# Kernel tuning notes

Hardware: AMD Instinct MI355X
Metric: run time of the kernel (lower is better)

## Reference

```python
import jax, jax.numpy as jnp
import numpy as np


def setup_inputs() -> dict:
    key = jax.random.key(0)
    k1, k2, k3, k4 = jax.random.split(key, 4)
    B, N, F, T, K, O = 16, 1024, 16, 12, 3, 16
    x = jax.random.normal(k1, (B, N, F, T), dtype=jnp.float32)
    spatial_attention = jax.random.uniform(k2, (B, N, N), dtype=jnp.float32)
    adj = jax.random.uniform(k3, (N, N), dtype=jnp.float32)
    # xavier_uniform_ on [K, F, O]: bound = sqrt(6/(F+O)) over last two dims
    bound = float(np.sqrt(6.0 / (F + O)))
    Theta = jax.random.uniform(k4, (K, F, O), dtype=jnp.float32, minval=-bound, maxval=bound)
    return {"x": x, "spatial_attention": spatial_attention, "adj": adj, "Theta": Theta}


def reference(x, spatial_attention, adj, Theta):
    # x: [B, N, F, T], spatial_attention: [B, N, N], adj: [N, N], Theta: [K, F, O]
    B, N, F, T = x.shape
    K = Theta.shape[0]
    a = adj[None, :, :] * spatial_attention                      # [B, N, N]
    eye = jnp.broadcast_to(jnp.eye(N, dtype=x.dtype), (B, N, N))
    supports = [eye, a]
    for _ in range(2, K):                                        # power series of adjacency
        supports.append(jnp.matmul(supports[-1], a))
    S = jnp.stack(supports, axis=0)                              # [K, B, N, N]
    # rhs[k,b,n,f,t] = sum_m S[k,b,m,n] * x[b,m,f,t]  (supports[k]^T @ x), fused over T and K
    rhs = jnp.einsum('kbmn,bmft->kbnft', S, x)                   # [K, B, N, F, T]
    out = jnp.einsum('kbnft,kfo->bnot', rhs, Theta)              # [B, N, O, T]
    return jax.nn.relu(out)
```

## Files before the change

### kernel.cpp

```cpp
#include <hip/hip_runtime.h>
#include <hip/hip_bf16.h>


typedef __attribute__((ext_vector_type(8))) __bf16 bf16x8;
typedef __attribute__((ext_vector_type(4))) float  f32x4;
typedef __attribute__((ext_vector_type(8))) short  short8;

__device__ inline unsigned short f32_to_bf16(float f) {
    unsigned int u = __builtin_bit_cast(unsigned int, f);
    unsigned int r = u + 0x7FFFu + ((u >> 16) & 1u);
    return (unsigned short)(r >> 16);
}
__device__ inline float bf16_to_f32(unsigned short u) {
    unsigned int x = ((unsigned int)u) << 16;
    return __builtin_bit_cast(float, x);
}

__global__ void prep_a(const float* __restrict__ sa, const float* __restrict__ adj,
                       unsigned short* __restrict__ aT)
{
    __shared__ float tile[32][33];
    const int b  = blockIdx.z;
    const int m0 = blockIdx.y * 32;
    const int n0 = blockIdx.x * 32;
    const int tid = threadIdx.x;
    const int c  = tid & 31;
    const int r4 = tid >> 5;
    const float* sab = sa + (size_t)b * 1024 * 1024;
#pragma unroll
    for (int i = 0; i < 4; i++) {
        int rr = r4 + i * 8;
        size_t idx = (size_t)(m0 + rr) * 1024 + (n0 + c);
        tile[rr][c] = adj[idx] * sab[idx];
    }
    __syncthreads();
    unsigned short* aTb = aT + (size_t)b * 1024 * 1024;
#pragma unroll
    for (int i = 0; i < 4; i++) {
        int rr = r4 + i * 8;
        aTb[(size_t)(n0 + rr) * 1024 + (m0 + c)] = f32_to_bf16(tile[c][rr]);
    }
}

__global__ void prep_x(const float* __restrict__ x, unsigned short* __restrict__ xT)
{
    __shared__ float tile[32][33];
    const int b  = blockIdx.z;
    const int j0 = blockIdx.y * 32;
    const int m0 = blockIdx.x * 32;
    const int tid = threadIdx.x;
    const int c  = tid & 31;
    const int r4 = tid >> 5;
    const float* xb = x + (size_t)b * 1024 * 192;
#pragma unroll
    for (int i = 0; i < 4; i++) {
        int rr = r4 + i * 8;
        tile[rr][c] = xb[(size_t)(m0 + rr) * 192 + (j0 + c)];
    }
    __syncthreads();
    unsigned short* xTb = xT + (size_t)b * 192 * 1024;
#pragma unroll
    for (int i = 0; i < 4; i++) {
        int rr = r4 + i * 8;
        xTb[(size_t)(j0 + rr) * 1024 + (m0 + c)] = f32_to_bf16(tile[c][rr]);
    }
}

#define GEMM_BJ 96
#define GEMM_BN 128
#define GEMM_BK 64
#define LDS_STRIDE 72

__global__ __launch_bounds__(256, 2)
void gemm_tn(const unsigned short* __restrict__ Aop,
             const unsigned short* __restrict__ Bop,
             unsigned short* __restrict__ Cout)
{
    const int b  = blockIdx.z;
    const int j0 = blockIdx.y * GEMM_BJ;
    const int n0 = blockIdx.x * GEMM_BN;
    const unsigned short* Ab = Aop + (size_t)b * 192 * 1024;
    const unsigned short* Bb = Bop + (size_t)b * 1024 * 1024;

    __shared__ unsigned short Alds[GEMM_BJ][LDS_STRIDE];
    __shared__ unsigned short Blds[GEMM_BN][LDS_STRIDE];

    const int tid  = threadIdx.x;
    const int lane = tid & 63;
    const int wave = tid >> 6;
    const int wj   = wave >> 1;
    const int wn   = wave & 1;
    const int lr   = lane & 15;
    const int lk   = (lane >> 4) * 8;

    f32x4 acc[3][4];
#pragma unroll
    for (int i = 0; i < 3; i++)
#pragma unroll
        for (int j = 0; j < 4; j++) acc[i][j] = f32x4{0.f, 0.f, 0.f, 0.f};

    for (int m0 = 0; m0 < 1024; m0 += GEMM_BK) {
        short8 aval[3], bval[4];
#pragma unroll
        for (int i = 0; i < 3; i++) {
            int id = tid + i * 256, r = id >> 3, c = id & 7;
            aval[i] = *reinterpret_cast<const short8*>(Ab + (size_t)(j0 + r) * 1024 + m0 + c * 8);
        }
#pragma unroll
        for (int i = 0; i < 4; i++) {
            int id = tid + i * 256, r = id >> 3, c = id & 7;
            bval[i] = *reinterpret_cast<const short8*>(Bb + (size_t)(n0 + r) * 1024 + m0 + c * 8);
        }
        __syncthreads();
#pragma unroll
        for (int i = 0; i < 3; i++) {
            int id = tid + i * 256, r = id >> 3, c = id & 7;
            *reinterpret_cast<short8*>(&Alds[r][c * 8]) = aval[i];
        }
#pragma unroll
        for (int i = 0; i < 4; i++) {
            int id = tid + i * 256, r = id >> 3, c = id & 7;
            *reinterpret_cast<short8*>(&Blds[r][c * 8]) = bval[i];
        }
        __syncthreads();
#pragma unroll
        for (int kk = 0; kk < GEMM_BK; kk += 32) {
            bf16x8 af[3], bfr[4];
#pragma unroll
            for (int ri = 0; ri < 3; ri++)
                af[ri] = __builtin_bit_cast(bf16x8,
                    *reinterpret_cast<const short8*>(&Alds[wj * 48 + ri * 16 + lr][kk + lk]));
#pragma unroll
            for (int ci = 0; ci < 4; ci++)
                bfr[ci] = __builtin_bit_cast(bf16x8,
                    *reinterpret_cast<const short8*>(&Blds[wn * 64 + ci * 16 + lr][kk + lk]));
#pragma unroll
            for (int ri = 0; ri < 3; ri++)
#pragma unroll
                for (int ci = 0; ci < 4; ci++)
                    acc[ri][ci] = __builtin_amdgcn_mfma_f32_16x16x32_bf16(
                        af[ri], bfr[ci], acc[ri][ci], 0, 0, 0);
        }
    }
    unsigned short* Cb = Cout + (size_t)b * 192 * 1024;
    const int jw = j0 + wj * 48;
    const int nw = n0 + wn * 64;
#pragma unroll
    for (int ri = 0; ri < 3; ri++)
#pragma unroll
        for (int ci = 0; ci < 4; ci++) {
            int col = nw + ci * 16 + lr;
#pragma unroll
            for (int r = 0; r < 4; r++) {
                int row = jw + ri * 16 + (lane >> 4) * 4 + r;
                Cb[(size_t)row * 1024 + col] = f32_to_bf16(acc[ri][ci][r]);
            }
        }
}

__global__ __launch_bounds__(256)
void final_contract(const unsigned short* __restrict__ xT,
                    const unsigned short* __restrict__ r1,
                    const unsigned short* __restrict__ r2,
                    const float* __restrict__ Theta,
                    float* __restrict__ out)
{
    __shared__ float th[3][16][16];
    const int tid = threadIdx.x;
    for (int i = tid; i < 768; i += 256) ((float*)th)[i] = Theta[i];
    __syncthreads();

    const int gid = blockIdx.x * 256 + tid;
    const int n   = gid & 1023;
    const int btq = gid >> 10;
    const int tq  = btq % 3;
    const int b   = btq / 3;
    const size_t base = (size_t)b * 192 * 1024 + n;

    float acc[4][16];
#pragma unroll
    for (int tt = 0; tt < 4; tt++)
#pragma unroll
        for (int o = 0; o < 16; o++) acc[tt][o] = 0.f;

#pragma unroll
    for (int f = 0; f < 16; f++) {
        size_t off = base + (size_t)(f * 12 + tq * 4) * 1024;
        float v0[4], v1[4], v2[4];
#pragma unroll
        for (int tt = 0; tt < 4; tt++) {
            v0[tt] = bf16_to_f32(xT[off + (size_t)tt * 1024]);
            v1[tt] = bf16_to_f32(r1[off + (size_t)tt * 1024]);
            v2[tt] = bf16_to_f32(r2[off + (size_t)tt * 1024]);
        }
        const f32x4* t0 = reinterpret_cast<const f32x4*>(&th[0][f][0]);
        const f32x4* t1 = reinterpret_cast<const f32x4*>(&th[1][f][0]);
        const f32x4* t2 = reinterpret_cast<const f32x4*>(&th[2][f][0]);
#pragma unroll
        for (int q = 0; q < 4; q++) {
            f32x4 w0 = t0[q], w1 = t1[q], w2 = t2[q];
#pragma unroll
            for (int tt = 0; tt < 4; tt++)
#pragma unroll
                for (int e = 0; e < 4; e++)
                    acc[tt][q * 4 + e] += v0[tt] * w0[e] + v1[tt] * w1[e] + v2[tt] * w2[e];
        }
    }
    float* outp = out + ((size_t)(b * 1024 + n) * 16) * 12 + tq * 4;
#pragma unroll
    for (int o = 0; o < 16; o++) {
        f32x4 v;
#pragma unroll
        for (int tt = 0; tt < 4; tt++) v[tt] = fmaxf(acc[tt][o], 0.f);
        *reinterpret_cast<f32x4*>(&outp[o * 12]) = v;
    }
}

extern "C" void kernel_launch(void* const* d_in, const int* in_sizes, int n_in,
                              void* d_out, int out_size, void* d_ws, size_t ws_size,
                              hipStream_t stream)
{
    const float* x     = (const float*)d_in[0];
    const float* sa    = (const float*)d_in[1];
    const float* adj   = (const float*)d_in[2];
    const float* Theta = (const float*)d_in[3];
    float* out = (float*)d_out;

    char* ws = (char*)d_ws;
    const size_t SZ_AT = (size_t)16 * 1024 * 1024 * 2;
    const size_t SZ_XT = (size_t)16 * 192  * 1024 * 2;
    unsigned short* aT = (unsigned short*)ws;
    unsigned short* xT = (unsigned short*)(ws + SZ_AT);
    unsigned short* r1 = (unsigned short*)(ws + SZ_AT + SZ_XT);
    unsigned short* r2 = (unsigned short*)(ws + SZ_AT + 2 * SZ_XT);

    prep_a<<<dim3(32, 32, 16), 256, 0, stream>>>(sa, adj, aT);
    prep_x<<<dim3(32, 6, 16), 256, 0, stream>>>(x, xT);
    gemm_tn<<<dim3(8, 2, 16), 256, 0, stream>>>(xT, aT, r1);
    gemm_tn<<<dim3(8, 2, 16), 256, 0, stream>>>(r1, aT, r2);
    final_contract<<<dim3(192), 256, 0, stream>>>(xT, r1, r2, Theta, out);
}
```

Measured before the change: 85.18 us.

## Double-buffer GEMM with direct global-to-LDS loads and stage output via LDS

The batched GEMM now streams the adjacency operand into double-buffered, XOR-swizzled LDS using global_load_lds, and keeps the A operand in registers loaded straight from global memory with prefetch of the next K-step. This removes the register round trip and one barrier per iteration. The N tile drops from 128 to 64, doubling the grid. The final contraction is regrouped per 64 nodes and stages its ReLU output in LDS so it can write fully coalesced f32x4 stores. The cost is 48KB of LDS in final_contract, one idle wave out of four there, and more redundant A-operand loads per GEMM block.

```diff
diff --git a/kernel.cpp b/kernel.cpp
--- a/kernel.cpp
+++ b/kernel.cpp
@@ -14,6 +14,13 @@
 __device__ inline float bf16_to_f32(unsigned short u) {
     unsigned int x = ((unsigned int)u) << 16;
     return __builtin_bit_cast(float, x);
+}
+
+__device__ inline void gload_lds16(const void* gsrc, void* ldst) {
+    __builtin_amdgcn_global_load_lds(
+        (const __attribute__((address_space(1))) unsigned int*)gsrc,
+        (__attribute__((address_space(3))) unsigned int*)ldst,
+        16, 0, 0);
 }
 
 __global__ void prep_a(const float* __restrict__ sa, const float* __restrict__ adj,
@@ -66,24 +73,18 @@
     }
 }
 
-#define GEMM_BJ 96
-#define GEMM_BN 128
-#define GEMM_BK 64
-#define LDS_STRIDE 72
-
 __global__ __launch_bounds__(256, 2)
 void gemm_tn(const unsigned short* __restrict__ Aop,
              const unsigned short* __restrict__ Bop,
              unsigned short* __restrict__ Cout)
 {
     const int b  = blockIdx.z;
-    const int j0 = blockIdx.y * GEMM_BJ;
-    const int n0 = blockIdx.x * GEMM_BN;
+    const int j0 = blockIdx.y * 96;
+    const int n0 = blockIdx.x * 64;
     const unsigned short* Ab = Aop + (size_t)b * 192 * 1024;
     const unsigned short* Bb = Bop + (size_t)b * 1024 * 1024;
 
-    __shared__ unsigned short Alds[GEMM_BJ][LDS_STRIDE];
-    __shared__ unsigned short Blds[GEMM_BN][LDS_STRIDE];
+    __shared__ unsigned short Blds[2][64 * 64];
 
     const int tid  = threadIdx.x;
     const int lane = tid & 63;
@@ -91,64 +92,93 @@
     const int wj   = wave >> 1;
     const int wn   = wave & 1;
     const int lr   = lane & 15;
-    const int lk   = (lane >> 4) * 8;
-
-    f32x4 acc[3][4];
+    const int lk8  = (lane >> 4) * 8;
+
+    const int srow = lane >> 3;
+    const int sg16 = (lane & 7) ^ srow;
+    const int sc0  = wave * 2;
+
+    f32x4 acc[3][2];
 #pragma unroll
     for (int i = 0; i < 3; i++)
 #pragma unroll
-        for (int j = 0; j < 4; j++) acc[i][j] = f32x4{0.f, 0.f, 0.f, 0.f};
-
-    for (int m0 = 0; m0 < 1024; m0 += GEMM_BK) {
-        short8 aval[3], bval[4];
-#pragma unroll
-        for (int i = 0; i < 3; i++) {
-            int id = tid + i * 256, r = id >> 3, c = id & 7;
-            aval[i] = *reinterpret_cast<const short8*>(Ab + (size_t)(j0 + r) * 1024 + m0 + c * 8);
-        }
-#pragma unroll
-        for (int i = 0; i < 4; i++) {
-            int id = tid + i * 256, r = id >> 3, c = id & 7;
-            bval[i] = *reinterpret_cast<const short8*>(Bb + (size_t)(n0 + r) * 1024 + m0 + c * 8);
-        }
+        for (int j = 0; j < 2; j++) acc[i][j] = f32x4{0.f, 0.f, 0.f, 0.f};
+
+    const unsigned short* Arow[3];
+#pragma unroll
+    for (int ri = 0; ri < 3; ri++)
+        Arow[ri] = Ab + (size_t)(j0 + wj * 48 + ri * 16 + lr) * 1024 + lk8;
+
+    bf16x8 Ac[2][3], An[2][3];
+
+#pragma unroll
+    for (int i = 0; i < 2; i++) {
+        int c = sc0 + i;
+        gload_lds16(Bb + (size_t)(n0 + 8 * c + srow) * 1024 + sg16 * 8,
+                    &Blds[0][c * 512]);
+    }
+#pragma unroll
+    for (int h = 0; h < 2; h++)
+#pragma unroll
+        for (int ri = 0; ri < 3; ri++)
+            Ac[h][ri] = __builtin_bit_cast(bf16x8,
+                *reinterpret_cast<const short8*>(Arow[ri] + h * 32));
+    __syncthreads();
+
+    int cur = 0;
+    for (int t = 0; t < 16; ++t) {
+        const int m0 = t * 64;
+        if (t < 15) {
+#pragma unroll
+            for (int i = 0; i < 2; i++) {
+                int c = sc0 + i;
+                gload_lds16(Bb + (size_t)(n0 + 8 * c + srow) * 1024 + (m0 + 64) + sg16 * 8,
+                            &Blds[cur ^ 1][c * 512]);
+            }
+#pragma unroll
+            for (int h = 0; h < 2; h++)
+#pragma unroll
+                for (int ri = 0; ri < 3; ri++)
+                    An[h][ri] = __builtin_bit_cast(bf16x8,
+                        *reinterpret_cast<const short8*>(Arow[ri] + m0 + 64 + h * 32));
+        }
+        bf16x8 Bfr[2][2];
+        const char* base = (const char*)&Blds[cur][0];
+#pragma unroll
+        for (int h = 0; h < 2; h++)
+#pragma unroll
+            for (int ci = 0; ci < 2; ci++) {
+                int row = wn * 32 + ci * 16 + lr;
+                int c16 = (h * 32 + lk8) >> 3;
+                int sw  = c16 ^ (row & 7);
+                Bfr[h][ci] = __builtin_bit_cast(bf16x8,
+                    *reinterpret_cast<const short8*>(base + row * 128 + sw * 16));
+            }
+#pragma unroll
+        for (int h = 0; h < 2; h++)
+#pragma unroll
+            for (int ri = 0; ri < 3; ri++)
+#pragma unroll
+                for (int ci = 0; ci < 2; ci++)
+                    acc[ri][ci] = __builtin_amdgcn_mfma_f32_16x16x32_bf16(
+                        Ac[h][ri], Bfr[h][ci], acc[ri][ci], 0, 0, 0);
         __syncthreads();
-#pragma unroll
-        for (int i = 0; i < 3; i++) {
-            int id = tid + i * 256, r = id >> 3, c = id & 7;
-            *reinterpret_cast<short8*>(&Alds[r][c * 8]) = aval[i];
-        }
-#pragma unroll
-        for (int i = 0; i < 4; i++) {
-            int id = tid + i * 256, r = id >> 3, c = id & 7;
-            *reinterpret_cast<short8*>(&Blds[r][c * 8]) = bval[i];
-        }
-        __syncthreads();
-#pragma unroll
-        for (int kk = 0; kk < GEMM_BK; kk += 32) {
-            bf16x8 af[3], bfr[4];
-#pragma unroll
-            for (int ri = 0; ri < 3; ri++)
-                af[ri] = __builtin_bit_cast(bf16x8,
-                    *reinterpret_cast<const short8*>(&Alds[wj * 48 + ri * 16 + lr][kk + lk]));
-#pragma unroll
-            for (int ci = 0; ci < 4; ci++)
-                bfr[ci] = __builtin_bit_cast(bf16x8,
-                    *reinterpret_cast<const short8*>(&Blds[wn * 64 + ci * 16 + lr][kk + lk]));
-#pragma unroll
-            for (int ri = 0; ri < 3; ri++)
-#pragma unroll
-                for (int ci = 0; ci < 4; ci++)
-                    acc[ri][ci] = __builtin_amdgcn_mfma_f32_16x16x32_bf16(
-                        af[ri], bfr[ci], acc[ri][ci], 0, 0, 0);
-        }
-    }
+        if (t < 15) {
+#pragma unroll
+            for (int h = 0; h < 2; h++)
+#pragma unroll
+                for (int ri = 0; ri < 3; ri++) Ac[h][ri] = An[h][ri];
+            cur ^= 1;
+        }
+    }
+
     unsigned short* Cb = Cout + (size_t)b * 192 * 1024;
     const int jw = j0 + wj * 48;
-    const int nw = n0 + wn * 64;
+    const int nw = n0 + wn * 32;
 #pragma unroll
     for (int ri = 0; ri < 3; ri++)
 #pragma unroll
-        for (int ci = 0; ci < 4; ci++) {
+        for (int ci = 0; ci < 2; ci++) {
             int col = nw + ci * 16 + lr;
 #pragma unroll
             for (int r = 0; r < 4; r++) {
@@ -165,55 +195,63 @@
                     const float* __restrict__ Theta,
                     float* __restrict__ out)
 {
-    __shared__ float th[3][16][16];
+    __shared__ float th[768];
+    __shared__ float obuf[64 * 192];
+
     const int tid = threadIdx.x;
-    for (int i = tid; i < 768; i += 256) ((float*)th)[i] = Theta[i];
-    __syncthreads();
-
-    const int gid = blockIdx.x * 256 + tid;
-    const int n   = gid & 1023;
-    const int btq = gid >> 10;
-    const int tq  = btq % 3;
-    const int b   = btq / 3;
-    const size_t base = (size_t)b * 192 * 1024 + n;
-
-    float acc[4][16];
-#pragma unroll
-    for (int tt = 0; tt < 4; tt++)
-#pragma unroll
-        for (int o = 0; o < 16; o++) acc[tt][o] = 0.f;
-
-#pragma unroll
-    for (int f = 0; f < 16; f++) {
-        size_t off = base + (size_t)(f * 12 + tq * 4) * 1024;
-        float v0[4], v1[4], v2[4];
-#pragma unroll
-        for (int tt = 0; tt < 4; tt++) {
-            v0[tt] = bf16_to_f32(xT[off + (size_t)tt * 1024]);
-            v1[tt] = bf16_to_f32(r1[off + (size_t)tt * 1024]);
-            v2[tt] = bf16_to_f32(r2[off + (size_t)tt * 1024]);
-        }
-        const f32x4* t0 = reinterpret_cast<const f32x4*>(&th[0][f][0]);
-        const f32x4* t1 = reinterpret_cast<const f32x4*>(&th[1][f][0]);
-        const f32x4* t2 = reinterpret_cast<const f32x4*>(&th[2][f][0]);
-#pragma unroll
-        for (int q = 0; q < 4; q++) {
-            f32x4 w0 = t0[q], w1 = t1[q], w2 = t2[q];
+    for (int i = tid; i < 768; i += 256) th[i] = Theta[i];
+    __syncthreads();
+
+    const int b  = blockIdx.y;
+    const int n0 = blockIdx.x * 64;
+    const int nl = tid & 63;
+    const int tq = tid >> 6;
+
+    if (tq < 3) {
+        float acc[4][16];
+#pragma unroll
+        for (int tt = 0; tt < 4; tt++)
+#pragma unroll
+            for (int o = 0; o < 16; o++) acc[tt][o] = 0.f;
+
+        const size_t basep = (size_t)b * 192 * 1024 + n0 + nl;
+#pragma unroll
+        for (int f = 0; f < 16; f++) {
+            size_t off = basep + (size_t)(f * 12 + tq * 4) * 1024;
+            float v0[4], v1[4], v2[4];
+#pragma unroll
+            for (int tt = 0; tt < 4; tt++) {
+                v0[tt] = bf16_to_f32(xT[off + (size_t)tt * 1024]);
+                v1[tt] = bf16_to_f32(r1[off + (size_t)tt * 1024]);
+                v2[tt] = bf16_to_f32(r2[off + (size_t)tt * 1024]);
+            }
+            const f32x4* t0 = reinterpret_cast<const f32x4*>(&th[0 * 256 + f * 16]);
+            const f32x4* t1 = reinterpret_cast<const f32x4*>(&th[1 * 256 + f * 16]);
+            const f32x4* t2 = reinterpret_cast<const f32x4*>(&th[2 * 256 + f * 16]);
+#pragma unroll
+            for (int q = 0; q < 4; q++) {
+                f32x4 w0 = t0[q], w1 = t1[q], w2 = t2[q];
+#pragma unroll
+                for (int tt = 0; tt < 4; tt++)
+#pragma unroll
+                    for (int e = 0; e < 4; e++)
+                        acc[tt][q * 4 + e] += v0[tt] * w0[e] + v1[tt] * w1[e] + v2[tt] * w2[e];
+            }
+        }
+#pragma unroll
+        for (int o = 0; o < 16; o++)
 #pragma unroll
             for (int tt = 0; tt < 4; tt++)
-#pragma unroll
-                for (int e = 0; e < 4; e++)
-                    acc[tt][q * 4 + e] += v0[tt] * w0[e] + v1[tt] * w1[e] + v2[tt] * w2[e];
-        }
-    }
-    float* outp = out + ((size_t)(b * 1024 + n) * 16) * 12 + tq * 4;
-#pragma unroll
-    for (int o = 0; o < 16; o++) {
-        f32x4 v;
-#pragma unroll
-        for (int tt = 0; tt < 4; tt++) v[tt] = fmaxf(acc[tt][o], 0.f);
-        *reinterpret_cast<f32x4*>(&outp[o * 12]) = v;
-    }
+                obuf[nl * 192 + o * 12 + tq * 4 + tt] = fmaxf(acc[tt][o], 0.f);
+    }
+    __syncthreads();
+
+    float* outp = out + ((size_t)b * 1024 + n0) * 192;
+    const f32x4* src = reinterpret_cast<const f32x4*>(obuf);
+    f32x4* dst = reinterpret_cast<f32x4*>(outp);
+#pragma unroll
+    for (int i = 0; i < 12; i++)
+        dst[tid + i * 256] = src[tid + i * 256];
 }
 
 extern "C" void kernel_launch(void* const* d_in, const int* in_sizes, int n_in,
@@ -236,7 +274,7 @@
 
     prep_a<<<dim3(32, 32, 16), 256, 0, stream>>>(sa, adj, aT);
     prep_x<<<dim3(32, 6, 16), 256, 0, stream>>>(x, xT);
-    gemm_tn<<<dim3(8, 2, 16), 256, 0, stream>>>(xT, aT, r1);
-    gemm_tn<<<dim3(8, 2, 16), 256, 0, stream>>>(r1, aT, r2);
-    final_contract<<<dim3(192), 256, 0, stream>>>(xT, r1, r2, Theta, out);
-}
+    gemm_tn<<<dim3(16, 2, 16), 256, 0, stream>>>(xT, aT, r1);
+    gemm_tn<<<dim3(16, 2, 16), 256, 0, stream>>>(r1, aT, r2);
+    final_contract<<<dim3(16, 16), 256, 0, stream>>>(xT, r1, r2, Theta, out);
+}
```

After: 95.57 us. 12.2% more time.
